# Performance work log

Hardware: AMD Instinct MI355X
Metric: run time of the kernel (lower is better)

Reference implementation:

```python
import jax, jax.numpy as jnp
import numpy as np

B, T, D, H = 2, 2048, 1024, 16
DH = D // H


def setup_inputs() -> dict:
    key = jax.random.key(0)
    ks = jax.random.split(key, 11)
    s = 1.0 / np.sqrt(D)
    return {
        "q": jax.random.normal(ks[0], (B, T, D), jnp.float32),
        "k": jax.random.normal(ks[1], (B, T, D), jnp.float32),
        "v": jax.random.normal(ks[2], (B, T, D), jnp.float32),
        "wq_w": jax.random.normal(ks[3], (D, D), jnp.float32) * s,
        "wq_b": jnp.zeros((D,), jnp.float32),
        "wk_w": jax.random.normal(ks[4], (D, D), jnp.float32) * s,
        "wk_b": jnp.zeros((D,), jnp.float32),
        "wv_w": jax.random.normal(ks[5], (D, D), jnp.float32) * s,
        "wv_b": jnp.zeros((D,), jnp.float32),
        "wo_w": jax.random.normal(ks[6], (D, D), jnp.float32) * s,
        "wo_b": jnp.zeros((D,), jnp.float32),
    }


def reference(q, k, v, wq_w, wq_b, wk_w, wk_b, wv_w, wv_b, wo_w, wo_b):
    b, t, d = q.shape
    # Linear projections (torch Linear: x @ W^T + b)
    wq = (q @ wq_w.T + wq_b).reshape(b, t, H, DH)
    wk = (k @ wk_w.T + wk_b).reshape(b, t, H, DH)
    wv = (v @ wv_w.T + wv_b).reshape(b, t, H, DH)
    # scaled dot-product attention: [b,h,t,s]
    scores = jnp.einsum('bthd,bshd->bhts', wq, wk) / jnp.sqrt(jnp.float32(DH))
    probs = jax.nn.softmax(scores, axis=-1)
    attn = jnp.einsum('bhts,bshd->bthd', probs, wv)  # [b,t,h,dh]
    attn = attn.reshape(b, t, d)
    return attn @ wo_w.T + wo_b
```

## Files before the change

### kernel.cpp

```cpp
#include <hip/hip_runtime.h>
#include <hip/hip_bf16.h>
#include <stdint.h>

#define Bn  2
#define Tn  2048
#define Dn  1024
#define Hn  16
#define DHn 64
#define Mn  (Bn*Tn)

typedef __attribute__((ext_vector_type(8))) short short8;
typedef __attribute__((ext_vector_type(4))) short short4v;
typedef __attribute__((ext_vector_type(4))) float f32x4;

__device__ __forceinline__ f32x4 fzero4() { f32x4 z = {0.f, 0.f, 0.f, 0.f}; return z; }

#define TR16(dst, a32) asm volatile("ds_read_b64_tr_b16 %0, %1" : "=v"(dst) : "v"(a32))

__global__ void cvt3_kernel(const float* __restrict__ a0, const float* __restrict__ a1,
                            const float* __restrict__ a2,
                            __hip_bfloat16* __restrict__ o0, __hip_bfloat16* __restrict__ o1,
                            __hip_bfloat16* __restrict__ o2, int n)
{
    const int i = (blockIdx.x * blockDim.x + threadIdx.x) * 8;
    if (i >= n) return;
    const float* in = blockIdx.y == 0 ? a0 : (blockIdx.y == 1 ? a1 : a2);
    __hip_bfloat16* out = blockIdx.y == 0 ? o0 : (blockIdx.y == 1 ? o1 : o2);
    float4 a = *(const float4*)(in + i);
    float4 b = *(const float4*)(in + i + 4);
    union { __hip_bfloat16 h[8]; short8 u; } tmp;
    tmp.h[0] = __float2bfloat16(a.x); tmp.h[1] = __float2bfloat16(a.y);
    tmp.h[2] = __float2bfloat16(a.z); tmp.h[3] = __float2bfloat16(a.w);
    tmp.h[4] = __float2bfloat16(b.x); tmp.h[5] = __float2bfloat16(b.y);
    tmp.h[6] = __float2bfloat16(b.z); tmp.h[7] = __float2bfloat16(b.w);
    *(short8*)(out + i) = tmp.u;
}

__global__ void cvt4_kernel(const float* __restrict__ a0, const float* __restrict__ a1,
                            const float* __restrict__ a2, const float* __restrict__ a3,
                            __hip_bfloat16* __restrict__ o0, __hip_bfloat16* __restrict__ o1,
                            __hip_bfloat16* __restrict__ o2, __hip_bfloat16* __restrict__ o3, int n)
{
    const int i = (blockIdx.x * blockDim.x + threadIdx.x) * 8;
    if (i >= n) return;
    const float* in = blockIdx.y == 0 ? a0 : (blockIdx.y == 1 ? a1 : (blockIdx.y == 2 ? a2 : a3));
    __hip_bfloat16* out = blockIdx.y == 0 ? o0 : (blockIdx.y == 1 ? o1 : (blockIdx.y == 2 ? o2 : o3));
    float4 a = *(const float4*)(in + i);
    float4 b = *(const float4*)(in + i + 4);
    union { __hip_bfloat16 h[8]; short8 u; } tmp;
    tmp.h[0] = __float2bfloat16(a.x); tmp.h[1] = __float2bfloat16(a.y);
    tmp.h[2] = __float2bfloat16(a.z); tmp.h[3] = __float2bfloat16(a.w);
    tmp.h[4] = __float2bfloat16(b.x); tmp.h[5] = __float2bfloat16(b.y);
    tmp.h[6] = __float2bfloat16(b.z); tmp.h[7] = __float2bfloat16(b.w);
    *(short8*)(out + i) = tmp.u;
}

__global__ __launch_bounds__(256, 2)
void gemm_qkv_kernel(const __hip_bfloat16* __restrict__ qa, const __hip_bfloat16* __restrict__ ka,
                     const __hip_bfloat16* __restrict__ va,
                     const __hip_bfloat16* __restrict__ wq, const __hip_bfloat16* __restrict__ wk,
                     const __hip_bfloat16* __restrict__ wv,
                     const float* __restrict__ bq_, const float* __restrict__ bk_,
                     const float* __restrict__ bv_,
                     __hip_bfloat16* __restrict__ Qp, __hip_bfloat16* __restrict__ Kp,
                     __hip_bfloat16* __restrict__ Vp)
{
    __shared__ alignas(16) short As[2][128*32];
    __shared__ alignas(16) short Bs[2][128*32];
    const int grp = blockIdx.y >> 3;
    const __hip_bfloat16* A  = grp == 0 ? qa : (grp == 1 ? ka : va);
    const __hip_bfloat16* Bw = grp == 0 ? wq : (grp == 1 ? wk : wv);
    const float* bias        = grp == 0 ? bq_ : (grp == 1 ? bk_ : bv_);
    __hip_bfloat16* C        = grp == 0 ? Qp : (grp == 1 ? Kp : Vp);

    const int t = threadIdx.x, lane = t & 63, wave = t >> 6;
    const int wm = wave >> 1, wn = wave & 1;
    const int row0 = blockIdx.x * 128, col0 = (blockIdx.y & 7) * 128;

    f32x4 acc[4][4];
#pragma unroll
    for (int m = 0; m < 4; ++m)
#pragma unroll
        for (int n = 0; n < 4; ++n) acc[m][n] = fzero4();

    const int srow = wave*16 + (lane >> 2);
    const int skk  = (lane & 3) * 8;
    const int ldsb = wave * 1024;

    auto STAGE = [&](int buf, int k0) {
#pragma unroll
        for (int i = 0; i < 2; ++i) {
            __builtin_amdgcn_global_load_lds(
                (const __attribute__((address_space(1))) void*)(A + (size_t)(row0 + i*64 + srow)*Dn + k0 + skk),
                (__attribute__((address_space(3))) void*)((char*)As[buf] + i*4096 + ldsb), 16, 0, 0);
            __builtin_amdgcn_global_load_lds(
                (const __attribute__((address_space(1))) void*)(Bw + (size_t)(col0 + i*64 + srow)*Dn + k0 + skk),
                (__attribute__((address_space(3))) void*)((char*)Bs[buf] + i*4096 + ldsb), 16, 0, 0);
        }
    };

    STAGE(0, 0);
    __syncthreads();
    int cur = 0;
    for (int k0 = 0; k0 < Dn; k0 += 32) {
        if (k0 + 32 < Dn) STAGE(cur ^ 1, k0 + 32);
        short8 af[4], bf_[4];
#pragma unroll
        for (int m = 0; m < 4; ++m)
            af[m] = *(const short8*)((char*)As[cur] + (wm*64 + m*16 + (lane & 15))*64 + (lane >> 4)*16);
#pragma unroll
        for (int n = 0; n < 4; ++n)
            bf_[n] = *(const short8*)((char*)Bs[cur] + (wn*64 + n*16 + (lane & 15))*64 + (lane >> 4)*16);
        __builtin_amdgcn_s_setprio(1);
#pragma unroll
        for (int m = 0; m < 4; ++m)
#pragma unroll
            for (int n = 0; n < 4; ++n)
                acc[m][n] = __builtin_amdgcn_mfma_f32_16x16x32_bf16(af[m], bf_[n], acc[m][n], 0, 0, 0);
        __builtin_amdgcn_s_setprio(0);
        __syncthreads();
        cur ^= 1;
    }

#pragma unroll
    for (int n = 0; n < 4; ++n) {
        const int col = col0 + wn*64 + n*16 + (lane & 15);
        const float bv = bias[col];
#pragma unroll
        for (int m = 0; m < 4; ++m) {
            const int rb_ = row0 + wm*64 + m*16 + (lane>>4)*4;
#pragma unroll
            for (int i = 0; i < 4; ++i)
                C[(size_t)(rb_+i)*Dn + col] = __float2bfloat16(acc[m][n][i] + bv);
        }
    }
}

__global__ __launch_bounds__(256, 2)
void gemm_out_kernel(const __hip_bfloat16* __restrict__ A,
                     const __hip_bfloat16* __restrict__ Bw,
                     const float* __restrict__ bias,
                     float* __restrict__ C)
{
    __shared__ alignas(16) short As[2][64*32];
    __shared__ alignas(16) short Bs[2][128*32];
    const int t = threadIdx.x, lane = t & 63, wave = t >> 6;
    const int wm = wave >> 1, wn = wave & 1;
    const int row0 = blockIdx.x * 64, col0 = blockIdx.y * 128;

    f32x4 acc[2][4];
#pragma unroll
    for (int m = 0; m < 2; ++m)
#pragma unroll
        for (int n = 0; n < 4; ++n) acc[m][n] = fzero4();

    const int srow = wave*16 + (lane >> 2);
    const int skk  = (lane & 3) * 8;
    const int ldsb = wave * 1024;

    auto STAGE = [&](int buf, int k0) {
        __builtin_amdgcn_global_load_lds(
            (const __attribute__((address_space(1))) void*)(A + (size_t)(row0 + srow)*Dn + k0 + skk),
            (__attribute__((address_space(3))) void*)((char*)As[buf] + ldsb), 16, 0, 0);
#pragma unroll
        for (int i = 0; i < 2; ++i)
            __builtin_amdgcn_global_load_lds(
                (const __attribute__((address_space(1))) void*)(Bw + (size_t)(col0 + i*64 + srow)*Dn + k0 + skk),
                (__attribute__((address_space(3))) void*)((char*)Bs[buf] + i*4096 + ldsb), 16, 0, 0);
    };

    STAGE(0, 0);
    __syncthreads();
    int cur = 0;
    for (int k0 = 0; k0 < Dn; k0 += 32) {
        if (k0 + 32 < Dn) STAGE(cur ^ 1, k0 + 32);
        short8 af[2], bf_[4];
#pragma unroll
        for (int m = 0; m < 2; ++m)
            af[m] = *(const short8*)((char*)As[cur] + (wm*32 + m*16 + (lane & 15))*64 + (lane >> 4)*16);
#pragma unroll
        for (int n = 0; n < 4; ++n)
            bf_[n] = *(const short8*)((char*)Bs[cur] + (wn*64 + n*16 + (lane & 15))*64 + (lane >> 4)*16);
        __builtin_amdgcn_s_setprio(1);
#pragma unroll
        for (int m = 0; m < 2; ++m)
#pragma unroll
            for (int n = 0; n < 4; ++n)
                acc[m][n] = __builtin_amdgcn_mfma_f32_16x16x32_bf16(af[m], bf_[n], acc[m][n], 0, 0, 0);
        __builtin_amdgcn_s_setprio(0);
        __syncthreads();
        cur ^= 1;
    }

#pragma unroll
    for (int n = 0; n < 4; ++n) {
        const int col = col0 + wn*64 + n*16 + (lane & 15);
        const float bv = bias[col];
#pragma unroll
        for (int m = 0; m < 2; ++m) {
            const int rb_ = row0 + wm*32 + m*16 + (lane>>4)*4;
#pragma unroll
            for (int i = 0; i < 4; ++i)
                C[(size_t)(rb_+i)*Dn + col] = acc[m][n][i] + bv;
        }
    }
}

#define VPL 1288

__device__ __forceinline__ void attn_step(
    const short8 (&ck)[4][2], const short8 (&cv)[2],
    short8 (&nk)[4][2], short8 (&nv)[2], int kvn, int buf,
    const short8 (&bq)[2][2], f32x4 (&o_)[2][4], float (&m_)[2], f32x4 (&lacc)[2],
    const __hip_bfloat16* K, const __hip_bfloat16* V, size_t base,
    int c, int g, int vrow, int vc, int vh, int vdst0, uint32_t atr, short* Vlds,
    const short8& ones)
{
    const float cexp = 0.18033688011112042f;

    {
        const __hip_bfloat16* kp = K + base + (size_t)(kvn + c) * Dn + g*8;
#pragma unroll
        for (int sub = 0; sub < 4; ++sub)
#pragma unroll
            for (int ks = 0; ks < 2; ++ks)
                nk[sub][ks] = *(const short8*)(kp + (size_t)sub*16*Dn + ks*32);
        const __hip_bfloat16* vp = V + base + (size_t)(kvn + vrow) * Dn + vc*16 + vh*8;
        nv[0] = *(const short8*)vp;
        nv[1] = *(const short8*)(vp + (size_t)32*Dn);
    }

    f32x4 s_[2][4];
#pragma unroll
    for (int qs = 0; qs < 2; ++qs)
#pragma unroll
        for (int sub = 0; sub < 4; ++sub) s_[qs][sub] = fzero4();
    __builtin_amdgcn_s_setprio(1);
#pragma unroll
    for (int qs = 0; qs < 2; ++qs)
#pragma unroll
        for (int sub = 0; sub < 4; ++sub)
#pragma unroll
            for (int ks = 0; ks < 2; ++ks)
                s_[qs][sub] = __builtin_amdgcn_mfma_f32_16x16x32_bf16(
                    ck[sub][ks], bq[qs][ks], s_[qs][sub], 0, 0, 0);
    __builtin_amdgcn_s_setprio(0);

    short8 pa[2][2];
#pragma unroll
    for (int qs = 0; qs < 2; ++qs) {
        float m01 = fmaxf(fmaxf(s_[qs][0][0], s_[qs][0][1]), fmaxf(s_[qs][0][2], s_[qs][0][3]));
        float m11 = fmaxf(fmaxf(s_[qs][1][0], s_[qs][1][1]), fmaxf(s_[qs][1][2], s_[qs][1][3]));
        float m21 = fmaxf(fmaxf(s_[qs][2][0], s_[qs][2][1]), fmaxf(s_[qs][2][2], s_[qs][2][3]));
        float m31 = fmaxf(fmaxf(s_[qs][3][0], s_[qs][3][1]), fmaxf(s_[qs][3][2], s_[qs][3][3]));
        float rm = fmaxf(fmaxf(m01, m11), fmaxf(m21, m31));
        rm = fmaxf(rm, __shfl_xor(rm, 16));
        rm = fmaxf(rm, __shfl_xor(rm, 32));
        if (!__all((rm - m_[qs]) * cexp <= 8.0f)) {
            const float mn = fmaxf(m_[qs], rm);
            const float sc = exp2f((m_[qs] - mn) * cexp);
            m_[qs] = mn;
#pragma unroll
            for (int i = 0; i < 4; ++i) lacc[qs][i] *= sc;
#pragma unroll
            for (int d = 0; d < 4; ++d)
#pragma unroll
                for (int i = 0; i < 4; ++i) o_[qs][d][i] *= sc;
        }
        const float mn = m_[qs];
#pragma unroll
        for (int kc = 0; kc < 2; ++kc)
#pragma unroll
            for (int hf = 0; hf < 2; ++hf)
#pragma unroll
                for (int i = 0; i < 4; ++i) {
                    const float p = exp2f((s_[qs][kc*2+hf][i] - mn) * cexp);
                    union { __hip_bfloat16 hb; short u; } cvp;
                    cvp.hb = __float2bfloat16(p);
                    pa[qs][kc][hf*4 + i] = cvp.u;
                }
        lacc[qs] = __builtin_amdgcn_mfma_f32_16x16x32_bf16(ones, pa[qs][0], lacc[qs], 0, 0, 0);
        lacc[qs] = __builtin_amdgcn_mfma_f32_16x16x32_bf16(ones, pa[qs][1], lacc[qs], 0, 0, 0);
    }

    short* vb = Vlds + buf*4*VPL;
    *(short8*)(&vb[vdst0])       = cv[0];
    *(short8*)(&vb[vdst0 + 640]) = cv[1];
    asm volatile("s_waitcnt lgkmcnt(0)" ::: "memory");
    __builtin_amdgcn_s_barrier();
    __builtin_amdgcn_sched_barrier(0);

    const uint32_t atrb = atr + (uint32_t)buf*10304u;
    short4v tv[4][2][2];
#pragma unroll
    for (int d = 0; d < 4; ++d)
#pragma unroll
        for (int kc = 0; kc < 2; ++kc) {
            const uint32_t a = atrb + (uint32_t)(d*2576 + kc*1280);
            TR16(tv[d][kc][0], a);
            TR16(tv[d][kc][1], a + 640);
        }
    asm volatile("s_waitcnt lgkmcnt(0)" ::: "memory");
    __builtin_amdgcn_sched_barrier(0);
    __builtin_amdgcn_s_setprio(1);
#pragma unroll
    for (int d = 0; d < 4; ++d) {
        const short8 av0 = __builtin_shufflevector(tv[d][0][0], tv[d][0][1], 0,1,2,3,4,5,6,7);
        const short8 av1 = __builtin_shufflevector(tv[d][1][0], tv[d][1][1], 0,1,2,3,4,5,6,7);
#pragma unroll
        for (int qs = 0; qs < 2; ++qs) {
            o_[qs][d] = __builtin_amdgcn_mfma_f32_16x16x32_bf16(av0, pa[qs][0], o_[qs][d], 0, 0, 0);
            o_[qs][d] = __builtin_amdgcn_mfma_f32_16x16x32_bf16(av1, pa[qs][1], o_[qs][d], 0, 0, 0);
        }
    }
    __builtin_amdgcn_s_setprio(0);
}

__global__ __launch_bounds__(256, 2)
void attn_kernel(const __hip_bfloat16* __restrict__ Q,
                 const __hip_bfloat16* __restrict__ K,
                 const __hip_bfloat16* __restrict__ V,
                 __hip_bfloat16* __restrict__ O)
{
    __shared__ alignas(16) short Vlds[2*4*VPL];
    const int t = threadIdx.x, lane = t & 63, wave = t >> 6;
    const int g = lane >> 4, c = lane & 15;
    const int blk = (blockIdx.x & 7) * 64 + (blockIdx.x >> 3);
    const int qb = blk & 15;
    const int h  = (blk >> 4) & (Hn - 1);
    const int b  = blk >> 8;
    const size_t base = (size_t)b * Tn * Dn + (size_t)h * DHn;
    const int q0 = qb * 128 + wave * 32;

    short8 bq[2][2];
#pragma unroll
    for (int qs = 0; qs < 2; ++qs) {
        const __hip_bfloat16* qp = Q + base + (size_t)(q0 + qs*16 + c) * Dn + g*8;
        bq[qs][0] = *(const short8*)qp;
        bq[qs][1] = *(const short8*)(qp + 32);
    }
    short8 ones;
#pragma unroll
    for (int i = 0; i < 8; ++i) ones[i] = (short)0x3F80;

    f32x4 o_[2][4];
#pragma unroll
    for (int qs = 0; qs < 2; ++qs)
#pragma unroll
        for (int d = 0; d < 4; ++d) o_[qs][d] = fzero4();
    float m_[2] = {-3e38f, -3e38f};
    f32x4 lacc[2] = {fzero4(), fzero4()};

    const int vrow = t >> 3;
    const int vc   = (t >> 1) & 3;
    const int vh   = t & 1;
    const int vdst0 = vc*VPL + (vrow>>2)*80 + (vrow&3)*16 + vh*8;
    const uint32_t vbase = (uint32_t)(uintptr_t)(void*)Vlds;
    const uint32_t atr = vbase + (uint32_t)(g*160 + c*8);

    short8 akA[4][2], akB[4][2], vrA[2], vrB[2];
    {
        const __hip_bfloat16* kp = K + base + (size_t)c * Dn + g*8;
#pragma unroll
        for (int sub = 0; sub < 4; ++sub)
#pragma unroll
            for (int ks = 0; ks < 2; ++ks)
                akA[sub][ks] = *(const short8*)(kp + (size_t)sub*16*Dn + ks*32);
        const __hip_bfloat16* vp = V + base + (size_t)vrow * Dn + vc*16 + vh*8;
        vrA[0] = *(const short8*)vp;
        vrA[1] = *(const short8*)(vp + (size_t)32*Dn);
    }

    for (int kv0 = 0; kv0 < Tn; kv0 += 128) {
        attn_step(akA, vrA, akB, vrB, kv0 + 64, 0, bq, o_, m_, lacc,
                  K, V, base, c, g, vrow, vc, vh, vdst0, atr, Vlds, ones);
        const int kvn = (kv0 + 128 < Tn) ? kv0 + 128 : 0;
        attn_step(akB, vrB, akA, vrA, kvn, 1, bq, o_, m_, lacc,
                  K, V, base, c, g, vrow, vc, vh, vdst0, atr, Vlds, ones);
    }

#pragma unroll
    for (int qs = 0; qs < 2; ++qs) {
        const float inv = 1.f / lacc[qs][0];
        __hip_bfloat16* op = O + base + (size_t)(q0 + qs*16 + c) * Dn + g*4;
#pragma unroll
        for (int d = 0; d < 4; ++d) {
            union { __hip_bfloat16 hb[4]; ushort4 u4; } w;
#pragma unroll
            for (int i = 0; i < 4; ++i) w.hb[i] = __float2bfloat16(o_[qs][d][i] * inv);
            *(ushort4*)(op + d*16) = w.u4;
        }
    }
}

extern "C" void kernel_launch(void* const* d_in, const int* in_sizes, int n_in,
                              void* d_out, int out_size, void* d_ws, size_t ws_size,
                              hipStream_t stream)
{
    (void)in_sizes; (void)n_in; (void)out_size; (void)ws_size;
    const float* q    = (const float*)d_in[0];
    const float* k    = (const float*)d_in[1];
    const float* v    = (const float*)d_in[2];
    const float* wq_w = (const float*)d_in[3];
    const float* wq_b = (const float*)d_in[4];
    const float* wk_w = (const float*)d_in[5];
    const float* wk_b = (const float*)d_in[6];
    const float* wv_w = (const float*)d_in[7];
    const float* wv_b = (const float*)d_in[8];
    const float* wo_w = (const float*)d_in[9];
    const float* wo_b = (const float*)d_in[10];

    char* ws = (char*)d_ws;
    const size_t S1 = (size_t)Mn * Dn * 2;
    const size_t W  = (size_t)Dn * Dn * 2;
    __hip_bfloat16* qb  = (__hip_bfloat16*)(ws);
    __hip_bfloat16* kb  = (__hip_bfloat16*)(ws + S1);
    __hip_bfloat16* vb  = (__hip_bfloat16*)(ws + 2*S1);
    __hip_bfloat16* wqb = (__hip_bfloat16*)(ws + 3*S1);
    __hip_bfloat16* wkb = (__hip_bfloat16*)(ws + 3*S1 + W);
    __hip_bfloat16* wvb = (__hip_bfloat16*)(ws + 3*S1 + 2*W);
    __hip_bfloat16* wob = (__hip_bfloat16*)(ws + 3*S1 + 3*W);
    __hip_bfloat16* Qp  = (__hip_bfloat16*)(ws + 3*S1 + 4*W);
    __hip_bfloat16* Kp  = (__hip_bfloat16*)(ws + 4*S1 + 4*W);
    __hip_bfloat16* Vp  = (__hip_bfloat16*)(ws + 5*S1 + 4*W);
    __hip_bfloat16* Ap  = (__hip_bfloat16*)(ws + 6*S1 + 4*W);

    const int nQKV = Mn * Dn;
    const int nW   = Dn * Dn;
    cvt3_kernel<<<dim3(nQKV/2048, 3), 256, 0, stream>>>(q, k, v, qb, kb, vb, nQKV);
    cvt4_kernel<<<dim3(nW/2048, 4), 256, 0, stream>>>(wq_w, wk_w, wv_w, wo_w,
                                                      wqb, wkb, wvb, wob, nW);

    gemm_qkv_kernel<<<dim3(Mn/128, 24), 256, 0, stream>>>(
        qb, kb, vb, wqb, wkb, wvb, wq_b, wk_b, wv_b, Qp, Kp, Vp);

    attn_kernel<<<Bn*Hn*(Tn/128), 256, 0, stream>>>(Qp, Kp, Vp, Ap);

    gemm_out_kernel<<<dim3(Mn/64, Dn/128), 256, 0, stream>>>(Ap, wob, wo_b, (float*)d_out);
}
```

Baseline: 150.9 us.

## Give each wave a private V LDS tile to remove block barriers

Each wave now stages the whole 64-row V tile itself into its own LDS region, so the per-step block-wide s_barrier and the shared double buffer go away. V loads move inside the step and are no longer prefetched a step ahead, and LDS use grows to four per-wave tiles. The transposed LDS reads are consumed with staggered lgkmcnt waits so PV MFMAs start before all reads finish. The row-max cross-lane shuffles now run only on the rescale path. Trade-offs: each wave does four times the V global loads, which hit L2, and V load latency is less hidden.

```diff
diff --git a/kernel.cpp b/kernel.cpp
--- a/kernel.cpp
+++ b/kernel.cpp
@@ -208,121 +208,13 @@
 
 #define VPL 1288
 
-__device__ __forceinline__ void attn_step(
-    const short8 (&ck)[4][2], const short8 (&cv)[2],
-    short8 (&nk)[4][2], short8 (&nv)[2], int kvn, int buf,
-    const short8 (&bq)[2][2], f32x4 (&o_)[2][4], float (&m_)[2], f32x4 (&lacc)[2],
-    const __hip_bfloat16* K, const __hip_bfloat16* V, size_t base,
-    int c, int g, int vrow, int vc, int vh, int vdst0, uint32_t atr, short* Vlds,
-    const short8& ones)
-{
-    const float cexp = 0.18033688011112042f;
-
-    {
-        const __hip_bfloat16* kp = K + base + (size_t)(kvn + c) * Dn + g*8;
-#pragma unroll
-        for (int sub = 0; sub < 4; ++sub)
-#pragma unroll
-            for (int ks = 0; ks < 2; ++ks)
-                nk[sub][ks] = *(const short8*)(kp + (size_t)sub*16*Dn + ks*32);
-        const __hip_bfloat16* vp = V + base + (size_t)(kvn + vrow) * Dn + vc*16 + vh*8;
-        nv[0] = *(const short8*)vp;
-        nv[1] = *(const short8*)(vp + (size_t)32*Dn);
-    }
-
-    f32x4 s_[2][4];
-#pragma unroll
-    for (int qs = 0; qs < 2; ++qs)
-#pragma unroll
-        for (int sub = 0; sub < 4; ++sub) s_[qs][sub] = fzero4();
-    __builtin_amdgcn_s_setprio(1);
-#pragma unroll
-    for (int qs = 0; qs < 2; ++qs)
-#pragma unroll
-        for (int sub = 0; sub < 4; ++sub)
-#pragma unroll
-            for (int ks = 0; ks < 2; ++ks)
-                s_[qs][sub] = __builtin_amdgcn_mfma_f32_16x16x32_bf16(
-                    ck[sub][ks], bq[qs][ks], s_[qs][sub], 0, 0, 0);
-    __builtin_amdgcn_s_setprio(0);
-
-    short8 pa[2][2];
-#pragma unroll
-    for (int qs = 0; qs < 2; ++qs) {
-        float m01 = fmaxf(fmaxf(s_[qs][0][0], s_[qs][0][1]), fmaxf(s_[qs][0][2], s_[qs][0][3]));
-        float m11 = fmaxf(fmaxf(s_[qs][1][0], s_[qs][1][1]), fmaxf(s_[qs][1][2], s_[qs][1][3]));
-        float m21 = fmaxf(fmaxf(s_[qs][2][0], s_[qs][2][1]), fmaxf(s_[qs][2][2], s_[qs][2][3]));
-        float m31 = fmaxf(fmaxf(s_[qs][3][0], s_[qs][3][1]), fmaxf(s_[qs][3][2], s_[qs][3][3]));
-        float rm = fmaxf(fmaxf(m01, m11), fmaxf(m21, m31));
-        rm = fmaxf(rm, __shfl_xor(rm, 16));
-        rm = fmaxf(rm, __shfl_xor(rm, 32));
-        if (!__all((rm - m_[qs]) * cexp <= 8.0f)) {
-            const float mn = fmaxf(m_[qs], rm);
-            const float sc = exp2f((m_[qs] - mn) * cexp);
-            m_[qs] = mn;
-#pragma unroll
-            for (int i = 0; i < 4; ++i) lacc[qs][i] *= sc;
-#pragma unroll
-            for (int d = 0; d < 4; ++d)
-#pragma unroll
-                for (int i = 0; i < 4; ++i) o_[qs][d][i] *= sc;
-        }
-        const float mn = m_[qs];
-#pragma unroll
-        for (int kc = 0; kc < 2; ++kc)
-#pragma unroll
-            for (int hf = 0; hf < 2; ++hf)
-#pragma unroll
-                for (int i = 0; i < 4; ++i) {
-                    const float p = exp2f((s_[qs][kc*2+hf][i] - mn) * cexp);
-                    union { __hip_bfloat16 hb; short u; } cvp;
-                    cvp.hb = __float2bfloat16(p);
-                    pa[qs][kc][hf*4 + i] = cvp.u;
-                }
-        lacc[qs] = __builtin_amdgcn_mfma_f32_16x16x32_bf16(ones, pa[qs][0], lacc[qs], 0, 0, 0);
-        lacc[qs] = __builtin_amdgcn_mfma_f32_16x16x32_bf16(ones, pa[qs][1], lacc[qs], 0, 0, 0);
-    }
-
-    short* vb = Vlds + buf*4*VPL;
-    *(short8*)(&vb[vdst0])       = cv[0];
-    *(short8*)(&vb[vdst0 + 640]) = cv[1];
-    asm volatile("s_waitcnt lgkmcnt(0)" ::: "memory");
-    __builtin_amdgcn_s_barrier();
-    __builtin_amdgcn_sched_barrier(0);
-
-    const uint32_t atrb = atr + (uint32_t)buf*10304u;
-    short4v tv[4][2][2];
-#pragma unroll
-    for (int d = 0; d < 4; ++d)
-#pragma unroll
-        for (int kc = 0; kc < 2; ++kc) {
-            const uint32_t a = atrb + (uint32_t)(d*2576 + kc*1280);
-            TR16(tv[d][kc][0], a);
-            TR16(tv[d][kc][1], a + 640);
-        }
-    asm volatile("s_waitcnt lgkmcnt(0)" ::: "memory");
-    __builtin_amdgcn_sched_barrier(0);
-    __builtin_amdgcn_s_setprio(1);
-#pragma unroll
-    for (int d = 0; d < 4; ++d) {
-        const short8 av0 = __builtin_shufflevector(tv[d][0][0], tv[d][0][1], 0,1,2,3,4,5,6,7);
-        const short8 av1 = __builtin_shufflevector(tv[d][1][0], tv[d][1][1], 0,1,2,3,4,5,6,7);
-#pragma unroll
-        for (int qs = 0; qs < 2; ++qs) {
-            o_[qs][d] = __builtin_amdgcn_mfma_f32_16x16x32_bf16(av0, pa[qs][0], o_[qs][d], 0, 0, 0);
-            o_[qs][d] = __builtin_amdgcn_mfma_f32_16x16x32_bf16(av1, pa[qs][1], o_[qs][d], 0, 0, 0);
-        }
-    }
-    __builtin_amdgcn_s_setprio(0);
-}
-
 __global__ __launch_bounds__(256, 2)
 void attn_kernel(const __hip_bfloat16* __restrict__ Q,
                  const __hip_bfloat16* __restrict__ K,
                  const __hip_bfloat16* __restrict__ V,
                  __hip_bfloat16* __restrict__ O)
 {
-    __shared__ alignas(16) short Vlds[2*4*VPL];
+    __shared__ alignas(16) short Vlds[4*4*VPL];
     const int t = threadIdx.x, lane = t & 63, wave = t >> 6;
     const int g = lane >> 4, c = lane & 15;
     const int blk = (blockIdx.x & 7) * 64 + (blockIdx.x >> 3);
@@ -331,6 +223,7 @@
     const int b  = blk >> 8;
     const size_t base = (size_t)b * Tn * Dn + (size_t)h * DHn;
     const int q0 = qb * 128 + wave * 32;
+    const float cexp = 0.18033688011112042f;
 
     short8 bq[2][2];
 #pragma unroll
@@ -351,14 +244,12 @@
     float m_[2] = {-3e38f, -3e38f};
     f32x4 lacc[2] = {fzero4(), fzero4()};
 
-    const int vrow = t >> 3;
-    const int vc   = (t >> 1) & 3;
-    const int vh   = t & 1;
-    const int vdst0 = vc*VPL + (vrow>>2)*80 + (vrow&3)*16 + vh*8;
+    short* vpriv = Vlds + wave*4*VPL;
+    const int vd_base = (lane>>2)*80 + (lane&3)*16;
     const uint32_t vbase = (uint32_t)(uintptr_t)(void*)Vlds;
-    const uint32_t atr = vbase + (uint32_t)(g*160 + c*8);
-
-    short8 akA[4][2], akB[4][2], vrA[2], vrB[2];
+    const uint32_t atr = vbase + (uint32_t)(wave*10304 + g*160 + c*8);
+
+    short8 akA[4][2], akB[4][2];
     {
         const __hip_bfloat16* kp = K + base + (size_t)c * Dn + g*8;
 #pragma unroll
@@ -366,17 +257,113 @@
 #pragma unroll
             for (int ks = 0; ks < 2; ++ks)
                 akA[sub][ks] = *(const short8*)(kp + (size_t)sub*16*Dn + ks*32);
-        const __hip_bfloat16* vp = V + base + (size_t)vrow * Dn + vc*16 + vh*8;
-        vrA[0] = *(const short8*)vp;
-        vrA[1] = *(const short8*)(vp + (size_t)32*Dn);
-    }
-
-    for (int kv0 = 0; kv0 < Tn; kv0 += 128) {
-        attn_step(akA, vrA, akB, vrB, kv0 + 64, 0, bq, o_, m_, lacc,
-                  K, V, base, c, g, vrow, vc, vh, vdst0, atr, Vlds, ones);
-        const int kvn = (kv0 + 128 < Tn) ? kv0 + 128 : 0;
-        attn_step(akB, vrB, akA, vrA, kvn, 1, bq, o_, m_, lacc,
-                  K, V, base, c, g, vrow, vc, vh, vdst0, atr, Vlds, ones);
+    }
+
+    auto STEP = [&](const short8 (&ck)[4][2], short8 (&nk)[4][2], int kvc, int kvn) {
+        short8 cv[8];
+        const __hip_bfloat16* vp = V + base + (size_t)(kvc + lane) * Dn;
+#pragma unroll
+        for (int u = 0; u < 8; ++u) cv[u] = *(const short8*)(vp + u*8);
+        {
+            const __hip_bfloat16* kp = K + base + (size_t)(kvn + c) * Dn + g*8;
+#pragma unroll
+            for (int sub = 0; sub < 4; ++sub)
+#pragma unroll
+                for (int ks = 0; ks < 2; ++ks)
+                    nk[sub][ks] = *(const short8*)(kp + (size_t)sub*16*Dn + ks*32);
+        }
+
+        f32x4 s_[2][4];
+#pragma unroll
+        for (int qs = 0; qs < 2; ++qs)
+#pragma unroll
+            for (int sub = 0; sub < 4; ++sub) s_[qs][sub] = fzero4();
+        __builtin_amdgcn_s_setprio(1);
+#pragma unroll
+        for (int qs = 0; qs < 2; ++qs)
+#pragma unroll
+            for (int sub = 0; sub < 4; ++sub)
+#pragma unroll
+                for (int ks = 0; ks < 2; ++ks)
+                    s_[qs][sub] = __builtin_amdgcn_mfma_f32_16x16x32_bf16(
+                        ck[sub][ks], bq[qs][ks], s_[qs][sub], 0, 0, 0);
+        __builtin_amdgcn_s_setprio(0);
+
+        short8 pa[2][2];
+#pragma unroll
+        for (int qs = 0; qs < 2; ++qs) {
+            float rm = s_[qs][0][0];
+#pragma unroll
+            for (int sub = 0; sub < 4; ++sub)
+#pragma unroll
+                for (int i = 0; i < 4; ++i) rm = fmaxf(rm, s_[qs][sub][i]);
+            if (!__all((rm - m_[qs]) * cexp <= 8.0f)) {
+                float gm = fmaxf(rm, __shfl_xor(rm, 16));
+                gm = fmaxf(gm, __shfl_xor(gm, 32));
+                const float mn = fmaxf(m_[qs], gm);
+                const float sc = exp2f((m_[qs] - mn) * cexp);
+                m_[qs] = mn;
+#pragma unroll
+                for (int i = 0; i < 4; ++i) lacc[qs][i] *= sc;
+#pragma unroll
+                for (int d = 0; d < 4; ++d)
+#pragma unroll
+                    for (int i = 0; i < 4; ++i) o_[qs][d][i] *= sc;
+            }
+            const float mn = m_[qs];
+#pragma unroll
+            for (int kc = 0; kc < 2; ++kc)
+#pragma unroll
+                for (int hf = 0; hf < 2; ++hf)
+#pragma unroll
+                    for (int i = 0; i < 4; ++i) {
+                        const float p = exp2f((s_[qs][kc*2+hf][i] - mn) * cexp);
+                        union { __hip_bfloat16 hb; short u; } cvp;
+                        cvp.hb = __float2bfloat16(p);
+                        pa[qs][kc][hf*4 + i] = cvp.u;
+                    }
+            lacc[qs] = __builtin_amdgcn_mfma_f32_16x16x32_bf16(ones, pa[qs][0], lacc[qs], 0, 0, 0);
+            lacc[qs] = __builtin_amdgcn_mfma_f32_16x16x32_bf16(ones, pa[qs][1], lacc[qs], 0, 0, 0);
+        }
+
+#pragma unroll
+        for (int u = 0; u < 8; ++u)
+            *(short8*)(vpriv + (u>>1)*VPL + vd_base + (u&1)*8) = cv[u];
+        asm volatile("s_waitcnt lgkmcnt(0)" ::: "memory");
+        __builtin_amdgcn_sched_barrier(0);
+
+        short4v tv[4][2][2];
+#pragma unroll
+        for (int d = 0; d < 4; ++d)
+#pragma unroll
+            for (int kc = 0; kc < 2; ++kc) {
+                const uint32_t a = atr + (uint32_t)(d*2576 + kc*1280);
+                TR16(tv[d][kc][0], a);
+                TR16(tv[d][kc][1], a + 640);
+            }
+#pragma unroll
+        for (int d = 0; d < 4; ++d) {
+            if (d == 0)      asm volatile("s_waitcnt lgkmcnt(12)" ::: "memory");
+            else if (d == 1) asm volatile("s_waitcnt lgkmcnt(8)" ::: "memory");
+            else if (d == 2) asm volatile("s_waitcnt lgkmcnt(4)" ::: "memory");
+            else             asm volatile("s_waitcnt lgkmcnt(0)" ::: "memory");
+            __builtin_amdgcn_sched_barrier(0);
+            const short8 av0 = __builtin_shufflevector(tv[d][0][0], tv[d][0][1], 0,1,2,3,4,5,6,7);
+            const short8 av1 = __builtin_shufflevector(tv[d][1][0], tv[d][1][1], 0,1,2,3,4,5,6,7);
+            __builtin_amdgcn_s_setprio(1);
+#pragma unroll
+            for (int qs = 0; qs < 2; ++qs) {
+                o_[qs][d] = __builtin_amdgcn_mfma_f32_16x16x32_bf16(av0, pa[qs][0], o_[qs][d], 0, 0, 0);
+                o_[qs][d] = __builtin_amdgcn_mfma_f32_16x16x32_bf16(av1, pa[qs][1], o_[qs][d], 0, 0, 0);
+            }
+            __builtin_amdgcn_s_setprio(0);
+        }
+    };
+
+    for (int it = 0; it < 16; ++it) {
+        const int kv0 = it * 128;
+        STEP(akA, akB, kv0, kv0 + 64);
+        STEP(akB, akA, kv0 + 64, (kv0 + 128) & (Tn - 1));
     }
 
 #pragma unroll
```

New measurement: 193.2 us. 1.28x slower.
